# Performance work log

Measured on AMD Instinct MI355X. Metric: run time of the kernel, lower is better.

## Reference

```python
import jax, jax.numpy as jnp
import numpy as np

# dims
B, QL, KL = 2, 1024, 4096
HID = 2048            # hidden_size
H, HD, RD = 16, 128, 64   # heads, head_dim, rope_dim
G = 4                 # gla_num_groups
HPG = H // G          # heads_per_group
QLR = 512             # q low-rank (W_dQ out)
LAT = 256             # latent_dim_per_group
KVP = G * LAT         # kv_proj_dim
EPS = 1e-6


def rmsnorm(x, w):
    var = jnp.mean(jnp.square(x.astype(jnp.float32)), axis=-1, keepdims=True)
    return (x * jax.lax.rsqrt(var + EPS)).astype(x.dtype) * w


def setup_inputs() -> dict:
    key = jax.random.key(0)
    ks = jax.random.split(key, 8)
    s = 0.02
    return {
        "x_q": jax.random.normal(ks[0], (B, QL, HID), jnp.float32),
        "x_kv": jax.random.normal(ks[1], (B, KL, HID), jnp.float32),
        "W_dQ": jax.random.normal(ks[2], (HID, QLR), jnp.float32) * s,
        "q_norm_w": jnp.ones((QLR,), jnp.float32),
        "W_uQ": jax.random.normal(ks[3], (QLR, H * (HD + RD)), jnp.float32) * s,
        "W_dKV": jax.random.normal(ks[4], (HID, KVP + RD), jnp.float32) * s,
        "kv_norm_w": jnp.ones((G, LAT), jnp.float32),
        "W_ukv": jax.random.normal(ks[5], (G, LAT, HPG * 2 * HD), jnp.float32) * s,
        "W_o": jax.random.normal(ks[6], (H * HD, HID), jnp.float32) * s,
    }


def reference(x_q, x_kv, W_dQ, q_norm_w, W_uQ, W_dKV, kv_norm_w, W_ukv, W_o):
    b, ql, _ = x_q.shape
    kl = x_kv.shape[1]
    # --- query path: down-proj -> RMSNorm -> up-proj -> drop rope dims ---
    q = rmsnorm(x_q @ W_dQ, q_norm_w)                       # [b, ql, QLR]
    q = (q @ W_uQ).reshape(b, ql, H, HD + RD)[..., :HD]     # [b, ql, H, HD]
    # --- kv path: down-proj -> slice -> per-group RMSNorm -> grouped up-proj ---
    ckv = (x_kv @ W_dKV)[..., :KVP].reshape(b, kl, G, LAT)  # [b, kl, G, LAT]
    ckv = rmsnorm(ckv, kv_norm_w)                           # weight [G, LAT] broadcasts
    kv = jnp.einsum("bsgl,gld->bsgd", ckv, W_ukv)           # [b, kl, G, HPG*2*HD]
    kv = kv.reshape(b, kl, H, 2 * HD)                       # group-major head order
    k, v = kv[..., :HD], kv[..., HD:]
    # --- SDPA (no mask, non-causal) ---
    scale = 1.0 / np.sqrt(HD).astype(np.float32)
    scores = jnp.einsum("bqhd,bkhd->bhqk", q, k) * scale    # [b, H, ql, kl]
    p = jax.nn.softmax(scores, axis=-1)
    out = jnp.einsum("bhqk,bkhd->bqhd", p, v).reshape(b, ql, H * HD)
    return out @ W_o
```

## Files before the change

kernel.cpp:

```cpp
#include <hip/hip_runtime.h>
#include <hip/hip_bf16.h>
#include <math.h>


typedef __attribute__((ext_vector_type(8))) short short8;
typedef __attribute__((ext_vector_type(4))) float f32x4;

__device__ __forceinline__ ushort f2bf(float x) {
    __hip_bfloat16 h = __float2bfloat16(x);
    return *reinterpret_cast<ushort*>(&h);
}

__device__ __forceinline__ void gl2lds16(const ushort* g, ushort* l) {
    __builtin_amdgcn_global_load_lds(
        (const __attribute__((address_space(1))) unsigned int*)g,
        (__attribute__((address_space(3))) unsigned int*)l, 16, 0, 0);
}

__global__ __launch_bounds__(256) void cast_bf16(const float* __restrict__ src,
        ushort* __restrict__ dst)
{
    size_t i = ((size_t)blockIdx.x * 256 + threadIdx.x) * 8;
    float4 a = *(const float4*)(src + i);
    float4 b = *(const float4*)(src + i + 4);
    ushort u[8] = {f2bf(a.x), f2bf(a.y), f2bf(a.z), f2bf(a.w),
                   f2bf(b.x), f2bf(b.y), f2bf(b.z), f2bf(b.w)};
    *(uint4*)(dst + i) = *(uint4*)u;
}

__global__ __launch_bounds__(256) void transpose_cast(const float* __restrict__ src,
        ushort* __restrict__ dst, int srl, int dstld, int remap,
        long src_z, long dst_z)
{
    __shared__ ushort tile[64][68];
    const int k0 = blockIdx.x * 64;
    const int n0 = blockIdx.y * 64;
    src += (size_t)blockIdx.z * src_z;
    dst += (size_t)blockIdx.z * dst_z;
    const int cb = n0 + (remap ? (n0 >> 7) * 64 : 0);
    const int t = threadIdx.x;
    {
        int r = t >> 4, c4 = t & 15;
        #pragma unroll
        for (int i = 0; i < 4; ++i) {
            float4 v = *(const float4*)(src + (size_t)(k0 + r + 16 * i) * srl + cb + c4 * 4);
            tile[r + 16 * i][c4 * 4 + 0] = f2bf(v.x);
            tile[r + 16 * i][c4 * 4 + 1] = f2bf(v.y);
            tile[r + 16 * i][c4 * 4 + 2] = f2bf(v.z);
            tile[r + 16 * i][c4 * 4 + 3] = f2bf(v.w);
        }
    }
    __syncthreads();
    {
        int n = t >> 4, k4 = t & 15;
        #pragma unroll
        for (int i = 0; i < 4; ++i) {
            ushort4 v;
            v.x = tile[k4 * 4 + 0][n + 16 * i];
            v.y = tile[k4 * 4 + 1][n + 16 * i];
            v.z = tile[k4 * 4 + 2][n + 16 * i];
            v.w = tile[k4 * 4 + 3][n + 16 * i];
            *(ushort4*)(dst + (size_t)(n0 + n + 16 * i) * dstld + k0 + k4 * 4) = v;
        }
    }
}

__global__ __launch_bounds__(256) void gemm_mfma(const ushort* __restrict__ A,
        const ushort* __restrict__ Bt, void* __restrict__ Cv,
        int M, int N, int K, int lda, int ldb, int ldc, int obf16, float scale,
        long strA, long strB, long strC)
{
    __shared__ ushort As[128 * 64];
    __shared__ ushort Bs[128 * 64];
    const int tid = threadIdx.x;
    const int w = tid >> 6, lane = tid & 63;
    const int quad = lane >> 4, l16 = lane & 15;
    const int wm = (w >> 1) * 64, wn = (w & 1) * 64;
    const int m0 = blockIdx.y * 128, n0 = blockIdx.x * 128;
    A  += (size_t)blockIdx.z * strA;
    Bt += (size_t)blockIdx.z * strB;

    f32x4 acc[4][4];
    #pragma unroll
    for (int i = 0; i < 4; ++i)
        #pragma unroll
        for (int j = 0; j < 4; ++j) acc[i][j] = (f32x4){0.f, 0.f, 0.f, 0.f};

    const int lr = lane >> 3;
    const int lc = (lane & 7) * 8;

    for (int k0 = 0; k0 < K; k0 += 64) {
        __syncthreads();
        #pragma unroll
        for (int i = 0; i < 4; ++i) {
            int r0 = w * 32 + i * 8;
            gl2lds16(A  + (size_t)(m0 + r0 + lr) * lda + k0 + lc, &As[r0 * 64]);
            gl2lds16(Bt + (size_t)(n0 + r0 + lr) * ldb + k0 + lc, &Bs[r0 * 64]);
        }
        __syncthreads();
        #pragma unroll
        for (int kc = 0; kc < 2; ++kc) {
            short8 af[4], bf[4];
            #pragma unroll
            for (int i = 0; i < 4; ++i) {
                af[i] = *(const short8*)&As[(wm + i * 16 + l16) * 64 + kc * 32 + quad * 8];
                bf[i] = *(const short8*)&Bs[(wn + i * 16 + l16) * 64 + kc * 32 + quad * 8];
            }
            #pragma unroll
            for (int i = 0; i < 4; ++i)
                #pragma unroll
                for (int j = 0; j < 4; ++j)
                    acc[i][j] = __builtin_amdgcn_mfma_f32_16x16x32_bf16(af[i], bf[j], acc[i][j], 0, 0, 0);
        }
    }
    if (!obf16) {
        float* C = (float*)Cv + (size_t)blockIdx.z * strC;
        #pragma unroll
        for (int i = 0; i < 4; ++i)
            #pragma unroll
            for (int r = 0; r < 4; ++r) {
                float* cp = C + (size_t)(m0 + wm + i * 16 + quad * 4 + r) * ldc + n0 + wn + l16;
                #pragma unroll
                for (int j = 0; j < 4; ++j) cp[j * 16] = acc[i][j][r] * scale;
            }
    } else {
        ushort* C = (ushort*)Cv + (size_t)blockIdx.z * strC;
        #pragma unroll
        for (int i = 0; i < 4; ++i)
            #pragma unroll
            for (int r = 0; r < 4; ++r) {
                ushort* cp = C + (size_t)(m0 + wm + i * 16 + quad * 4 + r) * ldc + n0 + wn + l16;
                #pragma unroll
                for (int j = 0; j < 4; ++j) cp[j * 16] = f2bf(acc[i][j][r] * scale);
            }
    }
}

__global__ __launch_bounds__(256) void rms_q_wave(const float* __restrict__ x,
        const float* __restrict__ w, ushort* __restrict__ dst)
{
    const int row = blockIdx.x * 4 + (threadIdx.x >> 6);
    const int lane = threadIdx.x & 63;
    const float* p = x + (size_t)row * 512;
    float4 v0 = *(const float4*)(p + lane * 4);
    float4 v1 = *(const float4*)(p + 256 + lane * 4);
    float ss = v0.x*v0.x + v0.y*v0.y + v0.z*v0.z + v0.w*v0.w
             + v1.x*v1.x + v1.y*v1.y + v1.z*v1.z + v1.w*v1.w;
    #pragma unroll
    for (int m = 1; m < 64; m <<= 1) ss += __shfl_xor(ss, m);
    float inv = rsqrtf(ss * (1.f / 512.f) + 1e-6f);
    float4 w0 = *(const float4*)(w + lane * 4);
    float4 w1 = *(const float4*)(w + 256 + lane * 4);
    ushort* dp = dst + (size_t)row * 512;
    ushort4 o0, o1;
    o0.x = f2bf(v0.x * inv * w0.x); o0.y = f2bf(v0.y * inv * w0.y);
    o0.z = f2bf(v0.z * inv * w0.z); o0.w = f2bf(v0.w * inv * w0.w);
    o1.x = f2bf(v1.x * inv * w1.x); o1.y = f2bf(v1.y * inv * w1.y);
    o1.z = f2bf(v1.z * inv * w1.z); o1.w = f2bf(v1.w * inv * w1.w);
    *(ushort4*)(dp + lane * 4)       = o0;
    *(ushort4*)(dp + 256 + lane * 4) = o1;
}

__global__ __launch_bounds__(256) void rms_kv_wave(const float* __restrict__ x,
        const float* __restrict__ w, ushort* __restrict__ dst)
{
    const int idx = blockIdx.x * 4 + (threadIdx.x >> 6);
    const int lane = threadIdx.x & 63;
    const int r = idx >> 2, g = idx & 3;
    const float* p = x + (size_t)r * 1024 + g * 256;
    float4 v = *(const float4*)(p + lane * 4);
    float ss = v.x*v.x + v.y*v.y + v.z*v.z + v.w*v.w;
    #pragma unroll
    for (int m = 1; m < 64; m <<= 1) ss += __shfl_xor(ss, m);
    float inv = rsqrtf(ss * (1.f / 256.f) + 1e-6f);
    float4 wv = *(const float4*)(w + g * 256 + lane * 4);
    ushort4 o;
    o.x = f2bf(v.x * inv * wv.x); o.y = f2bf(v.y * inv * wv.y);
    o.z = f2bf(v.z * inv * wv.z); o.w = f2bf(v.w * inv * wv.w);
    *(ushort4*)(dst + (size_t)r * 1024 + g * 256 + lane * 4) = o;
}

__global__ __launch_bounds__(256) void transpose_v(const ushort* __restrict__ KVb,
                                                   ushort* __restrict__ Vt)
{
    __shared__ ushort tile[64][66];
    const int s0 = blockIdx.x * 64;
    const int d0 = blockIdx.y * 64;
    const int bh = blockIdx.z;
    const int b = bh >> 4, h = bh & 15, g = h >> 2, p = h & 3;
    const int t = threadIdx.x;
    const ushort* src = KVb + (size_t)g * 8388608ull + (size_t)(b * 4096) * 1024 + p * 256 + 128;
    {
        int sl = t >> 4, c4 = t & 15;
        #pragma unroll
        for (int i = 0; i < 4; ++i) {
            int s = sl + 16 * i;
            ushort4 v = *(const ushort4*)(src + (size_t)(s0 + s) * 1024 + d0 + c4 * 4);
            tile[s][c4 * 4 + 0] = v.x; tile[s][c4 * 4 + 1] = v.y;
            tile[s][c4 * 4 + 2] = v.z; tile[s][c4 * 4 + 3] = v.w;
        }
    }
    __syncthreads();
    {
        int dl = t >> 4, s4 = t & 15;
        ushort* dst = Vt + (size_t)(b * 16 + h) * 128 * 4096;
        #pragma unroll
        for (int i = 0; i < 4; ++i) {
            int d = dl + 16 * i;
            ushort4 v;
            v.x = tile[s4 * 4 + 0][d]; v.y = tile[s4 * 4 + 1][d];
            v.z = tile[s4 * 4 + 2][d]; v.w = tile[s4 * 4 + 3][d];
            *(ushort4*)(dst + (size_t)(d0 + d) * 4096 + s0 + s4 * 4) = v;
        }
    }
}

__global__ __launch_bounds__(256) void attn_mfma_split(const ushort* __restrict__ Qb,
        const ushort* __restrict__ KVb, const ushort* __restrict__ Vt,
        float* __restrict__ Opart, float* __restrict__ ml)
{
    __shared__ ushort Ks[64][136];
    __shared__ ushort VsT[128][72];
    __shared__ ushort Ps[4][16][72];

    const int q0 = blockIdx.x * 64;
    const int h = blockIdx.y;
    const int b = blockIdx.z >> 1, chunk = blockIdx.z & 1;
    const int g = h >> 2, p = h & 3;
    const int tid = threadIdx.x;
    const int w = tid >> 6, lane = tid & 63;
    const int quad = lane >> 4, l16 = lane & 15;
    const int sbase = chunk * 2048;

    const ushort* qg = Qb + (size_t)(b * 1024 + q0) * 2048 + h * 128;
    const ushort* kg = KVb + (size_t)g * 8388608ull + (size_t)(b * 4096 + sbase) * 1024 + p * 256;
    const ushort* vg = Vt + (size_t)(b * 16 + h) * 128 * 4096 + sbase;

    {
        int r = tid >> 4, c8 = tid & 15;
        #pragma unroll
        for (int i = 0; i < 4; ++i)
            *(uint4*)&Ks[r + 16 * i][c8 * 8] =
                *(const uint4*)(qg + (size_t)(r + 16 * i) * 2048 + c8 * 8);
    }
    __syncthreads();
    short8 qf[4];
    {
        int qr = w * 16 + l16;
        #pragma unroll
        for (int kc = 0; kc < 4; ++kc)
            qf[kc] = *(const short8*)&Ks[qr][kc * 32 + quad * 8];
    }

    f32x4 accO[8];
    float m_i[4], l_i[4];
    #pragma unroll
    for (int dt = 0; dt < 8; ++dt) accO[dt] = (f32x4){0.f, 0.f, 0.f, 0.f};
    #pragma unroll
    for (int r = 0; r < 4; ++r) { m_i[r] = -INFINITY; l_i[r] = 0.f; }

    for (int s0 = 0; s0 < 2048; s0 += 64) {
        __syncthreads();
        {
            int r = tid >> 4, c8 = tid & 15;
            #pragma unroll
            for (int i = 0; i < 4; ++i)
                *(uint4*)&Ks[r + 16 * i][c8 * 8] =
                    *(const uint4*)(kg + (size_t)(s0 + r + 16 * i) * 1024 + c8 * 8);
            int d = tid >> 3, s8 = tid & 7;
            #pragma unroll
            for (int i = 0; i < 4; ++i)
                *(uint4*)&VsT[d + 32 * i][s8 * 8] =
                    *(const uint4*)(vg + (size_t)(d + 32 * i) * 4096 + s0 + s8 * 8);
        }
        __syncthreads();
        f32x4 accS[4];
        #pragma unroll
        for (int st = 0; st < 4; ++st) accS[st] = (f32x4){0.f, 0.f, 0.f, 0.f};
        #pragma unroll
        for (int kc = 0; kc < 4; ++kc) {
            #pragma unroll
            for (int st = 0; st < 4; ++st) {
                short8 kf = *(const short8*)&Ks[st * 16 + l16][kc * 32 + quad * 8];
                accS[st] = __builtin_amdgcn_mfma_f32_16x16x32_bf16(qf[kc], kf, accS[st], 0, 0, 0);
            }
        }
        #pragma unroll
        for (int r = 0; r < 4; ++r) {
            float tm = fmaxf(fmaxf(accS[0][r], accS[1][r]), fmaxf(accS[2][r], accS[3][r]));
            #pragma unroll
            for (int msk = 1; msk < 16; msk <<= 1) tm = fmaxf(tm, __shfl_xor(tm, msk));
            float mn = fmaxf(m_i[r], tm);
            float alpha = __expf(m_i[r] - mn);
            float rs = 0.f;
            #pragma unroll
            for (int st = 0; st < 4; ++st) {
                float e = __expf(accS[st][r] - mn);
                rs += e;
                Ps[w][quad * 4 + r][st * 16 + l16] = f2bf(e);
            }
            #pragma unroll
            for (int msk = 1; msk < 16; msk <<= 1) rs += __shfl_xor(rs, msk);
            l_i[r] = l_i[r] * alpha + rs;
            m_i[r] = mn;
            #pragma unroll
            for (int dt = 0; dt < 8; ++dt) accO[dt][r] *= alpha;
        }
        __syncthreads();
        short8 pf[2];
        #pragma unroll
        for (int sc = 0; sc < 2; ++sc)
            pf[sc] = *(const short8*)&Ps[w][l16][sc * 32 + quad * 8];
        #pragma unroll
        for (int sc = 0; sc < 2; ++sc) {
            #pragma unroll
            for (int dt = 0; dt < 8; ++dt) {
                short8 vf = *(const short8*)&VsT[dt * 16 + l16][sc * 32 + quad * 8];
                accO[dt] = __builtin_amdgcn_mfma_f32_16x16x32_bf16(pf[sc], vf, accO[dt], 0, 0, 0);
            }
        }
    }
    const int qrow = q0 + w * 16 + quad * 4;
    float* ob = Opart + (size_t)((chunk * 2 + b) * 1024 + qrow) * 2048 + h * 128 + l16;
    #pragma unroll
    for (int r = 0; r < 4; ++r)
        #pragma unroll
        for (int dt = 0; dt < 8; ++dt)
            ob[(size_t)r * 2048 + dt * 16] = accO[dt][r];
    if (l16 == 0) {
        #pragma unroll
        for (int r = 0; r < 4; ++r) {
            size_t mi = ((size_t)((chunk * 2 + b) * 1024 + qrow + r) * 16 + h) * 2;
            ml[mi] = m_i[r];
            ml[mi + 1] = l_i[r];
        }
    }
}

__global__ __launch_bounds__(256) void attn_merge(const float* __restrict__ Opart,
        const float* __restrict__ ml, ushort* __restrict__ Om)
{
    const int idx = blockIdx.x * 4 + (threadIdx.x >> 6);
    const int lane = threadIdx.x & 63;
    const int h = idx & 15;
    const int q = (idx >> 4) & 1023;
    const int b = idx >> 14;

    size_t m1i = ((size_t)((0 * 2 + b) * 1024 + q) * 16 + h) * 2;
    size_t m2i = ((size_t)((1 * 2 + b) * 1024 + q) * 16 + h) * 2;
    float m1 = ml[m1i], l1 = ml[m1i + 1];
    float m2 = ml[m2i], l2 = ml[m2i + 1];
    float M = fmaxf(m1, m2);
    float w1 = __expf(m1 - M), w2 = __expf(m2 - M);
    float invL = 1.f / (l1 * w1 + l2 * w2);

    const float* o1 = Opart + (size_t)((0 * 2 + b) * 1024 + q) * 2048 + h * 128;
    const float* o2 = Opart + (size_t)((1 * 2 + b) * 1024 + q) * 2048 + h * 128;
    ushort* ob = Om + (size_t)(b * 1024 + q) * 2048 + h * 128;
    ob[lane]      = f2bf((o1[lane]      * w1 + o2[lane]      * w2) * invL);
    ob[lane + 64] = f2bf((o1[lane + 64] * w1 + o2[lane + 64] * w2) * invL);
}

extern "C" void kernel_launch(void* const* d_in, const int* in_sizes, int n_in,
                              void* d_out, int out_size, void* d_ws, size_t ws_size,
                              hipStream_t stream)
{
    (void)in_sizes; (void)n_in; (void)out_size; (void)ws_size;
    const float* x_q       = (const float*)d_in[0];
    const float* x_kv      = (const float*)d_in[1];
    const float* W_dQ      = (const float*)d_in[2];
    const float* q_norm_w  = (const float*)d_in[3];
    const float* W_uQ      = (const float*)d_in[4];
    const float* W_dKV     = (const float*)d_in[5];
    const float* kv_norm_w = (const float*)d_in[6];
    const float* W_ukv     = (const float*)d_in[7];
    const float* W_o       = (const float*)d_in[8];
    float* out = (float*)d_out;

    float* ws = (float*)d_ws;
    ushort* xkvb       = (ushort*)ws;
    ushort* attn_out_b = (ushort*)ws;
    float*  mlbuf      = ws + 2097152ull;
    ushort* Wot        = (ushort*)(ws + 4194304ull);
    float*  ckv        = ws + 8388608ull;
    float*  Opart      = ws + 8388608ull;
    ushort* xqb        = (ushort*)(ws + 8388608ull);
    ushort* WdQt       = (ushort*)(ws + 10485760ull);
    float*  q_lat      = ws + 11010048ull;
    ushort* q_lat_b    = (ushort*)(ws + 12058624ull);
    ushort* WuQt       = (ushort*)(ws + 12582912ull);
    ushort* ckv_b      = (ushort*)(ws + 16777216ull);
    ushort* kvgb       = (ushort*)(ws + 20971520ull);
    ushort* vt         = (ushort*)(ws + 37748736ull);
    ushort* qb         = (ushort*)(ws + 46137344ull);
    ushort* WdKVt      = (ushort*)(ws + 48234496ull);
    ushort* Wukvt      = (ushort*)(ws + 49283072ull);

    const float qscale = 0.08838834764831845f;

    cast_bf16<<<2048, 256, 0, stream>>>(x_q, xqb);
    transpose_cast<<<dim3(32, 8, 1), 256, 0, stream>>>(W_dQ, WdQt, 512, 2048, 0, 0, 0);
    gemm_mfma<<<dim3(4, 16), 256, 0, stream>>>(xqb, WdQt, q_lat, 2048, 512, 2048, 2048, 2048, 512, 0, 1.f, 0, 0, 0);
    rms_q_wave<<<512, 256, 0, stream>>>(q_lat, q_norm_w, q_lat_b);
    transpose_cast<<<dim3(8, 32, 1), 256, 0, stream>>>(W_uQ, WuQt, 3072, 512, 1, 0, 0);
    gemm_mfma<<<dim3(16, 16), 256, 0, stream>>>(q_lat_b, WuQt, qb, 2048, 2048, 512, 512, 512, 2048, 1, qscale, 0, 0, 0);
    cast_bf16<<<8192, 256, 0, stream>>>(x_kv, xkvb);
    transpose_cast<<<dim3(32, 16, 1), 256, 0, stream>>>(W_dKV, WdKVt, 1088, 2048, 0, 0, 0);
    gemm_mfma<<<dim3(8, 64), 256, 0, stream>>>(xkvb, WdKVt, ckv, 8192, 1024, 2048, 2048, 2048, 1024, 0, 1.f, 0, 0, 0);
    rms_kv_wave<<<8192, 256, 0, stream>>>(ckv, kv_norm_w, ckv_b);
    transpose_cast<<<dim3(4, 16, 4), 256, 0, stream>>>(W_ukv, Wukvt, 1024, 256, 0, 262144, 262144);
    gemm_mfma<<<dim3(8, 64, 4), 256, 0, stream>>>(ckv_b, Wukvt, kvgb,
                                                  8192, 1024, 256, 1024, 256, 1024, 1, 1.f,
                                                  256, 262144, 8388608);
    transpose_v<<<dim3(64, 2, 32), 256, 0, stream>>>(kvgb, vt);
    attn_mfma_split<<<dim3(16, 16, 4), 256, 0, stream>>>(qb, kvgb, vt, Opart, mlbuf);
    attn_merge<<<8192, 256, 0, stream>>>(Opart, mlbuf, attn_out_b);
    transpose_cast<<<dim3(32, 32, 1), 256, 0, stream>>>(W_o, Wot, 2048, 2048, 0, 0, 0);
    gemm_mfma<<<dim3(16, 16), 256, 0, stream>>>(attn_out_b, Wot, out, 2048, 2048, 2048, 2048, 2048, 2048, 0, 1.f, 0, 0, 0);
}
```

Measured before the change: 567.9 us.

## Use DPP row reductions, padded GEMM LDS, remapped attention grid, drop barrier

```diff
diff --git a/kernel.cpp b/kernel.cpp
--- a/kernel.cpp
+++ b/kernel.cpp
@@ -11,10 +11,24 @@
     return *reinterpret_cast<ushort*>(&h);
 }
 
-__device__ __forceinline__ void gl2lds16(const ushort* g, ushort* l) {
-    __builtin_amdgcn_global_load_lds(
-        (const __attribute__((address_space(1))) unsigned int*)g,
-        (__attribute__((address_space(3))) unsigned int*)l, 16, 0, 0);
+template <int CTRL>
+__device__ __forceinline__ float dpp_ror(float x) {
+    return __int_as_float(__builtin_amdgcn_update_dpp(
+        0, __float_as_int(x), CTRL, 0xf, 0xf, true));
+}
+__device__ __forceinline__ float row_max16(float x) {
+    x = fmaxf(x, dpp_ror<0x128>(x));
+    x = fmaxf(x, dpp_ror<0x124>(x));
+    x = fmaxf(x, dpp_ror<0x122>(x));
+    x = fmaxf(x, dpp_ror<0x121>(x));
+    return x;
+}
+__device__ __forceinline__ float row_sum16(float x) {
+    x += dpp_ror<0x128>(x);
+    x += dpp_ror<0x124>(x);
+    x += dpp_ror<0x122>(x);
+    x += dpp_ror<0x121>(x);
+    return x;
 }
 
 __global__ __launch_bounds__(256) void cast_bf16(const float* __restrict__ src,
@@ -70,8 +84,8 @@
         int M, int N, int K, int lda, int ldb, int ldc, int obf16, float scale,
         long strA, long strB, long strC)
 {
-    __shared__ ushort As[128 * 64];
-    __shared__ ushort Bs[128 * 64];
+    __shared__ ushort As[128][72];
+    __shared__ ushort Bs[128][72];
     const int tid = threadIdx.x;
     const int w = tid >> 6, lane = tid & 63;
     const int quad = lane >> 4, l16 = lane & 15;
@@ -86,16 +100,16 @@
         #pragma unroll
         for (int j = 0; j < 4; ++j) acc[i][j] = (f32x4){0.f, 0.f, 0.f, 0.f};
 
-    const int lr = lane >> 3;
-    const int lc = (lane & 7) * 8;
+    const int str = tid >> 3;
+    const int stc = (tid & 7) * 8;
 
     for (int k0 = 0; k0 < K; k0 += 64) {
         __syncthreads();
         #pragma unroll
         for (int i = 0; i < 4; ++i) {
-            int r0 = w * 32 + i * 8;
-            gl2lds16(A  + (size_t)(m0 + r0 + lr) * lda + k0 + lc, &As[r0 * 64]);
-            gl2lds16(Bt + (size_t)(n0 + r0 + lr) * ldb + k0 + lc, &Bs[r0 * 64]);
+            int r = str + 32 * i;
+            *(uint4*)&As[r][stc] = *(const uint4*)(A + (size_t)(m0 + r) * lda + k0 + stc);
+            *(uint4*)&Bs[r][stc] = *(const uint4*)(Bt + (size_t)(n0 + r) * ldb + k0 + stc);
         }
         __syncthreads();
         #pragma unroll
@@ -103,8 +117,8 @@
             short8 af[4], bf[4];
             #pragma unroll
             for (int i = 0; i < 4; ++i) {
-                af[i] = *(const short8*)&As[(wm + i * 16 + l16) * 64 + kc * 32 + quad * 8];
-                bf[i] = *(const short8*)&Bs[(wn + i * 16 + l16) * 64 + kc * 32 + quad * 8];
+                af[i] = *(const short8*)&As[wm + i * 16 + l16][kc * 32 + quad * 8];
+                bf[i] = *(const short8*)&Bs[wn + i * 16 + l16][kc * 32 + quad * 8];
             }
             #pragma unroll
             for (int i = 0; i < 4; ++i)
@@ -223,9 +237,11 @@
     __shared__ ushort VsT[128][72];
     __shared__ ushort Ps[4][16][72];
 
-    const int q0 = blockIdx.x * 64;
-    const int h = blockIdx.y;
-    const int b = blockIdx.z >> 1, chunk = blockIdx.z & 1;
+    const int lid = blockIdx.x + 16 * (blockIdx.y + 16 * blockIdx.z);
+    const int q0 = (lid >> 6) * 64;
+    const int rem = lid & 63;
+    const int h = rem & 15;
+    const int b = (rem >> 5) & 1, chunk = (rem >> 4) & 1;
     const int g = h >> 2, p = h & 3;
     const int tid = threadIdx.x;
     const int w = tid >> 6, lane = tid & 63;
@@ -288,8 +304,7 @@
         #pragma unroll
         for (int r = 0; r < 4; ++r) {
             float tm = fmaxf(fmaxf(accS[0][r], accS[1][r]), fmaxf(accS[2][r], accS[3][r]));
-            #pragma unroll
-            for (int msk = 1; msk < 16; msk <<= 1) tm = fmaxf(tm, __shfl_xor(tm, msk));
+            tm = row_max16(tm);
             float mn = fmaxf(m_i[r], tm);
             float alpha = __expf(m_i[r] - mn);
             float rs = 0.f;
@@ -299,14 +314,12 @@
                 rs += e;
                 Ps[w][quad * 4 + r][st * 16 + l16] = f2bf(e);
             }
-            #pragma unroll
-            for (int msk = 1; msk < 16; msk <<= 1) rs += __shfl_xor(rs, msk);
+            rs = row_sum16(rs);
             l_i[r] = l_i[r] * alpha + rs;
             m_i[r] = mn;
             #pragma unroll
             for (int dt = 0; dt < 8; ++dt) accO[dt][r] *= alpha;
         }
-        __syncthreads();
         short8 pf[2];
         #pragma unroll
         for (int sc = 0; sc < 2; ++sc)
```

After: 640.9 us. +12.8%, slower.
